# Performance work log

Measured on AMD Instinct MI355X. Metric: run time of the kernel, lower is better.

## Reference

```python
import jax, jax.numpy as jnp
import numpy as np


def setup_inputs() -> dict:
    key = jax.random.key(0)
    k1, k2, k3 = jax.random.split(key, 3)
    B, N, M, D = 4, 1024, 2048, 9
    outputs = jax.random.normal(k1, (B, N, D), dtype=jnp.float32)
    targets = jax.random.normal(k2, (B, M, D), dtype=jnp.float32)
    mask = jax.random.randint(k3, (B, M), 0, 2).astype(bool)
    return {"outputs": outputs, "targets": targets, "mask": mask, "k": 64, "max_pair": 1024}


def reference(outputs, targets, mask, k, max_pair):
    # outputs: (B, N, 9), targets: (B, M, 9), mask: (B, M) bool
    y_pred = outputs[:, :max_pair]
    B, N, D = y_pred.shape
    M = targets.shape[1]

    # Statistics over masked ground-truth rows (weighted, jit-friendly)
    w = mask.astype(y_pred.dtype)            # (B, M)
    S = w.sum()                               # number of valid rows
    mean = jnp.einsum('bm,bmd->d', w, targets) / S               # (9,)
    centered = (targets - mean) * w[..., None]                    # (B, M, 9)
    cov = jnp.einsum('bmd,bme->de', centered, centered) / (S - 1.0)
    cov_inv = jnp.linalg.pinv(cov)                                # (9, 9)

    def maha(x):
        # NOTE: original code subtracts the GT mean from the pairwise
        # differences before the quadratic form -- kept faithfully.
        xc = x - mean
        return jnp.einsum('...i,ij,...j->...', xc, cov_inv, xc)

    def topk_smallest_per_col(d, kk):
        # d: (R, N); torch.topk(dim=0, largest=False) -> smallest kk per column
        return -jax.lax.top_k(-d.T, kk)[0]    # (N, kk)

    # Intra loss: GT-vs-pred pairwise distances, masked rows only
    diff = targets[:, :, None, :] - y_pred[:, None, :, :]          # (B, M, N, 9)
    Dn = maha(diff)                                                 # (B, M, N)
    Dn = jnp.where(mask[:, :, None], Dn, jnp.inf).reshape(B * M, N)
    intra_loss = topk_smallest_per_col(Dn, k).mean()

    # Inter (regularization) loss: pred-vs-pred pairwise
    # y_reg1_expand[b,i,j] = y_pred[b,j]; y_reg2_expand[b,i,j] = y_pred[b,i]
    diff_r = y_pred[:, None, :, :] - y_pred[:, :, None, :]          # (B, N, N, 9)
    Dr = maha(diff_r).reshape(B * N, N)
    inter_loss = topk_smallest_per_col(Dr, k).mean()

    return intra_loss - 0.1 * inter_loss
```

## Files before the change

### kernel.cpp

```cpp
#include <hip/hip_runtime.h>
#include <math.h>

#define B_ 4
#define N_ 1024
#define M_ 2048
#define D_ 9
#define K_ 64
#define BM_ (B_*M_)
#define BN_ (B_*N_)
#define TPRE_STRIDE 12
#define PPRE_STRIDE 12
#define NPART 32
#define NSTAT 55
#define TSEL 512
#define BUD 128

#define WS_A 0
#define WS_MEAN 81
#define WS_TPRE 96
#define WS_PPRE (WS_TPRE + BM_*TPRE_STRIDE)
#define WS_CS_INTRA (WS_PPRE + BN_*PPRE_STRIDE)
#define WS_CS_INTER (WS_CS_INTRA + N_)
#define WS_PART (WS_CS_INTER + N_)
#define WS_CANDI (WS_PART + NPART*(NSTAT+1))
#define WS_CANDE (WS_CANDI + 1024*2048)

__device__ __forceinline__ unsigned f2key(float f) {
  unsigned b = __float_as_uint(f);
  return (b & 0x80000000u) ? ~b : (b | 0x80000000u);
}
__device__ __forceinline__ float key2f(unsigned k) {
  unsigned b = (k & 0x80000000u) ? (k ^ 0x80000000u) : ~k;
  return __uint_as_float(b);
}

__device__ int detect_mask_fmt(const void* mask, int* flags ) {
  int tid = threadIdx.x;
  if (tid < 2) flags[tid] = 0;
  __syncthreads();
  const unsigned char* mb = (const unsigned char*)mask;
  int la = 0, lb = 0;
  for (int i = tid; i < BM_; i += blockDim.x) {
    unsigned char c = mb[i];
    if (c) { if (i & 3) la = 1; else if ((i & 7) == 4) lb = 1; }
  }
  if (la) atomicOr(&flags[0], 1);
  if (lb) atomicOr(&flags[1], 1);
  __syncthreads();
  return flags[0] ? 0 : (flags[1] ? 1 : 2);
}
__device__ __forceinline__ int mask_at(const void* mask, int fmt, int t) {
  if (fmt == 0) return ((const unsigned char*)mask)[t] != 0;
  if (fmt == 1) return ((const int*)mask)[t] != 0;
  return ((const long long*)mask)[t] != 0LL;
}

__global__ __launch_bounds__(256) void stats_part_kernel(
    const float* __restrict__ targets, const void* __restrict__ mask,
    float* __restrict__ ws) {
  __shared__ int flags[2];
  __shared__ float wpart[4][NSTAT];
  int tid = threadIdx.x;
  int fmt = detect_mask_fmt(mask, flags);
  int t = blockIdx.x * 256 + tid;

  float v[NSTAT];
  float tv[D_];
  int m = mask_at(mask, fmt, t);
  const float* tp = targets + t * D_;
#pragma unroll
  for (int d = 0; d < D_; ++d) tv[d] = m ? tp[d] : 0.f;
  v[0] = m ? 1.f : 0.f;
#pragma unroll
  for (int d = 0; d < D_; ++d) v[1 + d] = tv[d];
  {
    int p = 10;
#pragma unroll
    for (int i = 0; i < D_; ++i)
#pragma unroll
      for (int j = i; j < D_; ++j, ++p) v[p] = tv[i] * tv[j];
  }
#pragma unroll
  for (int off = 32; off > 0; off >>= 1)
#pragma unroll
    for (int p = 0; p < NSTAT; ++p) v[p] += __shfl_down(v[p], off);
  int wave = tid >> 6, lane = tid & 63;
  if (lane == 0)
#pragma unroll
    for (int p = 0; p < NSTAT; ++p) wpart[wave][p] = v[p];
  __syncthreads();
  if (tid < NSTAT) {
    float s = wpart[0][tid] + wpart[1][tid] + wpart[2][tid] + wpart[3][tid];
    ws[WS_PART + blockIdx.x * (NSTAT + 1) + tid] = s;
  }
}

__global__ __launch_bounds__(256) void pre_kernel(
    const float* __restrict__ outputs, const float* __restrict__ targets,
    const void* __restrict__ mask, float* __restrict__ ws) {
  __shared__ int flags[2];
  __shared__ float tot[NSTAT];
  __shared__ float Atmp[9][9];
  __shared__ float Ash[81];
  __shared__ float msh[D_];
  int tid = threadIdx.x;
  int fmt = detect_mask_fmt(mask, flags);
  if (tid < NSTAT) {
    double s = 0.0;
    for (int b = 0; b < NPART; ++b)
      s += (double)ws[WS_PART + b * (NSTAT + 1) + tid];
    tot[tid] = (float)s;
  }
  __syncthreads();
  if (tid < 64) {
    int lane = tid;
    float S = tot[0];
    float col[9];
    int j = lane - 9;
    if (lane < 9) {
      float mj = tot[1 + lane] / S;
#pragma unroll
      for (int r = 0; r < 9; ++r) {
        float mr = tot[1 + r] / S;
        int i0 = r < lane ? r : lane;
        int j0 = r < lane ? lane : r;
        int p = i0 * 9 - (i0 * (i0 - 1)) / 2 + (j0 - i0);
        col[r] = (tot[10 + p] - S * mr * mj) / (S - 1.0f);
      }
    } else {
#pragma unroll
      for (int r = 0; r < 9; ++r) col[r] = (r == j) ? 1.f : 0.f;
    }
#pragma unroll
    for (int c = 0; c < 9; ++c) {
      float pv = __shfl(col[c], c);
      float inv = 1.f / pv;
      col[c] *= inv;
      float f[9];
#pragma unroll
      for (int r = 0; r < 9; ++r) f[r] = __shfl(col[r], c);
#pragma unroll
      for (int r = 0; r < 9; ++r)
        if (r != c) col[r] -= f[r] * col[c];
    }
    if (lane >= 9 && lane < 18) {
#pragma unroll
      for (int r = 0; r < 9; ++r) Atmp[r][j] = col[r];
    }
  }
  __syncthreads();
  if (tid < 9) msh[tid] = tot[1 + tid] / tot[0];
  for (int idx = tid; idx < 81; idx += 256) {
    int i0 = idx / 9, j0 = idx % 9;
    Ash[idx] = 0.5f * (Atmp[i0][j0] + Atmp[j0][i0]);
  }
  __syncthreads();

  int idx = blockIdx.x * 256 + tid;
  if (idx < BM_) {
    const float* tp = targets + idx * D_;
    float u[D_];
#pragma unroll
    for (int d = 0; d < D_; ++d) u[d] = tp[d] - msh[d];
    float cu = 0.f; float au[D_];
#pragma unroll
    for (int i = 0; i < D_; ++i) {
      float s = 0.f;
#pragma unroll
      for (int j = 0; j < D_; ++j) s += Ash[i * D_ + j] * u[j];
      au[i] = s; cu += u[i] * s;
    }
    if (!mask_at(mask, fmt, idx)) cu = INFINITY;
    float* o = ws + WS_TPRE + idx * TPRE_STRIDE;
#pragma unroll
    for (int d = 0; d < D_; ++d) o[d] = au[d];
    o[9] = cu; o[10] = 0.f; o[11] = 0.f;
  } else if (idx < BM_ + BN_) {
    int r = idx - BM_;
    const float* yp = outputs + r * D_;
    float y[D_], q[D_], aq[D_];
#pragma unroll
    for (int d = 0; d < D_; ++d) { y[d] = yp[d]; q[d] = y[d] + msh[d]; }
    float cp = 0.f, cq = 0.f;
#pragma unroll
    for (int i = 0; i < D_; ++i) {
      float sy = 0.f, sq = 0.f;
#pragma unroll
      for (int j = 0; j < D_; ++j) {
        sy += Ash[i * D_ + j] * y[j];
        sq += Ash[i * D_ + j] * q[j];
      }
      cp += y[i] * sy;
      aq[i] = sq; cq += q[i] * sq;
    }
    float* o = ws + WS_PPRE + r * PPRE_STRIDE;
#pragma unroll
    for (int d = 0; d < D_; ++d) o[d] = aq[d];
    o[9] = cq; o[10] = cp; o[11] = 0.f;
  }
}

template <int PER>
__device__ __forceinline__ unsigned bisect64(const unsigned* key) {
  unsigned kmin = 0xFFFFFFFFu;
#pragma unroll
  for (int j = 0; j < PER; ++j) kmin = key[j] < kmin ? key[j] : kmin;
  unsigned gmin = kmin, mmax = kmin;
#pragma unroll
  for (int off = 32; off > 0; off >>= 1) {
    unsigned a = (unsigned)__shfl_xor((int)gmin, off);
    unsigned b = (unsigned)__shfl_xor((int)mmax, off);
    gmin = a < gmin ? a : gmin;
    mmax = b > mmax ? b : mmax;
  }
  unsigned lo = gmin, hi = mmax;
  while (lo < hi) {
    unsigned mid = lo + ((hi - lo) >> 1);
    int cnt = 0;
#pragma unroll
    for (int j = 0; j < PER; ++j) cnt += __popcll(__ballot(key[j] <= mid));
    if (cnt >= K_) hi = mid; else lo = mid + 1;
  }
  return lo;
}

template <int PER>
__device__ __forceinline__ void sel_thresh2(const unsigned* k0,
                                            const unsigned* k1,
                                            unsigned& T0o, unsigned& T1o,
                                            int& st0, int& st1) {
  unsigned mn0 = 0xFFFFFFFFu, mn1 = 0xFFFFFFFFu;
#pragma unroll
  for (int j = 0; j < PER; ++j) {
    mn0 = k0[j] < mn0 ? k0[j] : mn0;
    mn1 = k1[j] < mn1 ? k1[j] : mn1;
  }
  unsigned g0 = mn0, x0 = mn0, g1 = mn1, x1 = mn1;
#pragma unroll
  for (int off = 32; off > 0; off >>= 1) {
    unsigned a0 = (unsigned)__shfl_xor((int)g0, off);
    unsigned b0 = (unsigned)__shfl_xor((int)x0, off);
    unsigned a1 = (unsigned)__shfl_xor((int)g1, off);
    unsigned b1 = (unsigned)__shfl_xor((int)x1, off);
    g0 = a0 < g0 ? a0 : g0;  x0 = b0 > x0 ? b0 : x0;
    g1 = a1 < g1 ? a1 : g1;  x1 = b1 > x1 ? b1 : x1;
  }
  unsigned lo0 = g0, hi0 = x0, lo1 = g1, hi1 = x1;
  int c0 = 0, c1 = 0;
#pragma unroll
  for (int j = 0; j < PER; ++j) {
    c0 += __popcll(__ballot(k0[j] <= hi0));
    c1 += __popcll(__ballot(k1[j] <= hi1));
  }
  while (((lo0 < hi0) && (c0 > BUD)) || ((lo1 < hi1) && (c1 > BUD))) {
    int a0 = (lo0 < hi0) && (c0 > BUD);
    int a1 = (lo1 < hi1) && (c1 > BUD);
    unsigned mid0 = lo0 + ((hi0 - lo0) >> 1);
    unsigned mid1 = lo1 + ((hi1 - lo1) >> 1);
    int n0 = 0, n1 = 0;
#pragma unroll
    for (int j = 0; j < PER; ++j) {
      n0 += __popcll(__ballot(k0[j] <= mid0));
      n1 += __popcll(__ballot(k1[j] <= mid1));
    }
    if (a0) { if (n0 >= K_) { hi0 = mid0; c0 = n0; } else lo0 = mid0 + 1; }
    if (a1) { if (n1 >= K_) { hi1 = mid1; c1 = n1; } else lo1 = mid1 + 1; }
  }
  T0o = hi0; st0 = (c0 > BUD);
  T1o = hi1; st1 = (c1 > BUD);
}

template <int PER>
__device__ __forceinline__ void compactB(const unsigned* key, unsigned T,
                                         int strict, float* candw, int lane) {
  unsigned long long lmask = (1ull << lane) - 1ull;
  int n = 0;
#pragma unroll
  for (int j = 0; j < PER; ++j) {
    bool p = strict ? (key[j] < T) : (key[j] <= T);
    unsigned long long m = __ballot(p);
    if (p) candw[n + __popcll(m & lmask)] = key2f(key[j]);
    n += __popcll(m);
  }
  float tv = key2f(T);
  for (int i = n + lane; i < BUD; i += 64) candw[i] = tv;
}

template <int NP>
__device__ __forceinline__ float final_sum(const float* __restrict__ cand,
                                           int lane) {
  unsigned kk[NP];
#pragma unroll
  for (int j = 0; j < NP; ++j) kk[j] = f2key(cand[j * 64 + lane]);
  unsigned T = bisect64<NP>(kk);
  float s = 0.f; int c = 0;
#pragma unroll
  for (int j = 0; j < NP; ++j)
    if (kk[j] < T) { s += key2f(kk[j]); c++; }
#pragma unroll
  for (int off = 32; off > 0; off >>= 1) {
    s += __shfl_down(s, off);
    c += __shfl_down(c, off);
  }
  return s + (float)(K_ - c) * key2f(T);
}

__global__ __launch_bounds__(TSEL) void select_kernel(
    const float* __restrict__ outputs, const float* __restrict__ wsro,
    float* __restrict__ ws) {
  __shared__ float vsh[2][B_][D_];
  __shared__ float cvsh[2][B_];
  int tid = threadIdx.x, wave = tid >> 6, lane = tid & 63;
  int bid = blockIdx.x;
  int is_intra = bid < N_;
  int p = is_intra ? (bid >> 1) : (bid - N_);
  int h = is_intra ? (bid & 1) : 0;
  int c0 = 2 * p;
  if (tid < 2 * B_ * D_) {
    int c = tid / (B_ * D_), rem = tid % (B_ * D_), b = rem / D_, d = rem % D_;
    vsh[c][b][d] = outputs[(b * N_ + c0 + c) * D_ + d];
  }
  if (tid < 2 * B_) {
    int c = tid >> 2, b = tid & 3;
    cvsh[c][b] = wsro[WS_PPRE + (b * N_ + c0 + c) * PPRE_STRIDE + 10];
  }
  __syncthreads();
  constexpr int PER = 8;
  unsigned k0[PER], k1[PER];
  if (is_intra) {
    const float* pre = wsro + WS_TPRE;
    int rowbase = h * 4096;
#pragma unroll
    for (int bbb = 0; bbb < 2; ++bbb) {
      int b = 2 * h + bbb;
      float v0[D_], v1[D_];
#pragma unroll
      for (int d = 0; d < D_; ++d) { v0[d] = vsh[0][b][d]; v1[d] = vsh[1][b][d]; }
      float cv0 = cvsh[0][b], cv1 = cvsh[1][b];
#pragma unroll
      for (int jj = 0; jj < 4; ++jj) {
        int j = bbb * 4 + jj;
        const float* row = pre + (rowbase + tid + TSEL * j) * TPRE_STRIDE;
        float4 a0 = *(const float4*)row;
        float4 a1 = *(const float4*)(row + 4);
        float2 a2 = *(const float2*)(row + 8);
        float d0 = a0.x * v0[0] + a0.y * v0[1] + a0.z * v0[2] + a0.w * v0[3] +
                   a1.x * v0[4] + a1.y * v0[5] + a1.z * v0[6] + a1.w * v0[7] +
                   a2.x * v0[8];
        float d1 = a0.x * v1[0] + a0.y * v1[1] + a0.z * v1[2] + a0.w * v1[3] +
                   a1.x * v1[4] + a1.y * v1[5] + a1.z * v1[6] + a1.w * v1[7] +
                   a2.x * v1[8];
        k0[j] = f2key(a2.y + cv0 - 2.0f * d0);
        k1[j] = f2key(a2.y + cv1 - 2.0f * d1);
      }
      __builtin_amdgcn_sched_barrier(0);
    }
  } else {
    const float* pre = wsro + WS_PPRE;
#pragma unroll
    for (int bb = 0; bb < B_; ++bb) {
      float v0[D_], v1[D_];
#pragma unroll
      for (int d = 0; d < D_; ++d) { v0[d] = vsh[0][bb][d]; v1[d] = vsh[1][bb][d]; }
      float cv0 = cvsh[0][bb], cv1 = cvsh[1][bb];
#pragma unroll
      for (int jj = 0; jj < 2; ++jj) {
        int j = bb * 2 + jj;
        const float* row = pre + (tid + TSEL * j) * PPRE_STRIDE;
        float4 a0 = *(const float4*)row;
        float4 a1 = *(const float4*)(row + 4);
        float2 a2 = *(const float2*)(row + 8);
        float d0 = a0.x * v0[0] + a0.y * v0[1] + a0.z * v0[2] + a0.w * v0[3] +
                   a1.x * v0[4] + a1.y * v0[5] + a1.z * v0[6] + a1.w * v0[7] +
                   a2.x * v0[8];
        float d1 = a0.x * v1[0] + a0.y * v1[1] + a0.z * v1[2] + a0.w * v1[3] +
                   a1.x * v1[4] + a1.y * v1[5] + a1.z * v1[6] + a1.w * v1[7] +
                   a2.x * v1[8];
        k0[j] = f2key(a2.y + cv0 - 2.0f * d0);
        k1[j] = f2key(a2.y + cv1 - 2.0f * d1);
      }
      __builtin_amdgcn_sched_barrier(0);
    }
  }
  unsigned T0, T1; int st0, st1;
  sel_thresh2<PER>(k0, k1, T0, T1, st0, st1);
  if (is_intra) {
    compactB<PER>(k0, T0, st0,
                  ws + WS_CANDI + (c0) * 2048 + h * 1024 + wave * BUD, lane);
    compactB<PER>(k1, T1, st1,
                  ws + WS_CANDI + (c0 + 1) * 2048 + h * 1024 + wave * BUD, lane);
  } else {
    compactB<PER>(k0, T0, st0,
                  ws + WS_CANDE + (c0) * 1024 + wave * BUD, lane);
    compactB<PER>(k1, T1, st1,
                  ws + WS_CANDE + (c0 + 1) * 1024 + wave * BUD, lane);
  }
}

__global__ __launch_bounds__(512) void merge_kernel(
    const float* __restrict__ wsro, float* __restrict__ ws) {
  int gw = (blockIdx.x * 512 + threadIdx.x) >> 6;
  int lane = threadIdx.x & 63;
  if (gw < N_) {
    float s = final_sum<32>(wsro + WS_CANDI + gw * 2048, lane);
    if (lane == 0) ws[WS_CS_INTRA + gw] = s;
  } else {
    float s = final_sum<16>(wsro + WS_CANDE + (gw - N_) * 1024, lane);
    if (lane == 0) ws[WS_CS_INTER + (gw - N_)] = s;
  }
}

__global__ __launch_bounds__(256) void reduce_kernel(
    const float* __restrict__ ws, float* __restrict__ out) {
  __shared__ double sbuf[256];
  __shared__ double tA;
  int tid = threadIdx.x;
  double sa = 0.0, sb = 0.0;
  for (int i = tid; i < N_; i += 256) {
    sa += (double)ws[WS_CS_INTRA + i];
    sb += (double)ws[WS_CS_INTER + i];
  }
  sbuf[tid] = sa;
  __syncthreads();
  for (int off = 128; off > 0; off >>= 1) {
    if (tid < off) sbuf[tid] += sbuf[tid + off];
    __syncthreads();
  }
  if (tid == 0) tA = sbuf[0];
  __syncthreads();
  sbuf[tid] = sb;
  __syncthreads();
  for (int off = 128; off > 0; off >>= 1) {
    if (tid < off) sbuf[tid] += sbuf[tid + off];
    __syncthreads();
  }
  if (tid == 0) {
    double denom = (double)N_ * (double)K_;
    out[0] = (float)(tA / denom - 0.1 * (sbuf[0] / denom));
  }
}

extern "C" void kernel_launch(void* const* d_in, const int* in_sizes, int n_in,
                              void* d_out, int out_size, void* d_ws,
                              size_t ws_size, hipStream_t stream) {
  const float* outputs = (const float*)d_in[0];
  const float* targets = (const float*)d_in[1];
  const void* mask = d_in[2];
  float* ws = (float*)d_ws;

  hipLaunchKernelGGL(stats_part_kernel, dim3(NPART), dim3(256), 0, stream,
                     targets, mask, ws);
  hipLaunchKernelGGL(pre_kernel, dim3((BM_ + BN_ + 255) / 256), dim3(256), 0,
                     stream, outputs, targets, mask, ws);
  hipLaunchKernelGGL(select_kernel, dim3(N_ + N_ / 2), dim3(TSEL), 0, stream,
                     outputs, ws, ws);
  hipLaunchKernelGGL(merge_kernel, dim3(2 * N_ / 8), dim3(512), 0, stream,
                     ws, ws);
  hipLaunchKernelGGL(reduce_kernel, dim3(1), dim3(256), 0, stream, ws,
                     (float*)d_out);
}
```

Before: 70.79 us.

## Fuse candidate merge and final reduction into select kernel via LDS and atomics

The select kernel now keeps per-wave top-k candidates in shared memory and computes each column's final sum within the same block, so the separate merge and reduce kernels and the global candidate buffers go away. Each intra block now handles both batch halves in two serial passes instead of splitting them across two blocks. Column sums are accumulated in fixed-point 64-bit integer atomics, and the last block to finish writes the output. This removes two launches and the global round trip, but halves intra parallelism (1024 blocks instead of 1536) and adds atomic contention plus a fixed-point rounding change.

```diff
diff --git a/kernel.cpp b/kernel.cpp
--- a/kernel.cpp
+++ b/kernel.cpp
@@ -14,6 +14,7 @@
 #define NSTAT 55
 #define TSEL 512
 #define BUD 128
+#define NBLK 1024
 
 #define WS_A 0
 #define WS_MEAN 81
@@ -22,8 +23,7 @@
 #define WS_CS_INTRA (WS_PPRE + BN_*PPRE_STRIDE)
 #define WS_CS_INTER (WS_CS_INTRA + N_)
 #define WS_PART (WS_CS_INTER + N_)
-#define WS_CANDI (WS_PART + NPART*(NSTAT+1))
-#define WS_CANDE (WS_CANDI + 1024*2048)
+#define WS_ACC (WS_PART + NPART*(NSTAT+1))
 
 __device__ __forceinline__ unsigned f2key(float f) {
   unsigned b = __float_as_uint(f);
@@ -105,6 +105,10 @@
   __shared__ float msh[D_];
   int tid = threadIdx.x;
   int fmt = detect_mask_fmt(mask, flags);
+  if (blockIdx.x == 0 && tid == 0) {
+    long long* acc = (long long*)(ws + WS_ACC);
+    acc[0] = 0; acc[1] = 0; acc[2] = 0;
+  }
   if (tid < NSTAT) {
     double s = 0.0;
     for (int b = 0; b < NPART; ++b)
@@ -307,14 +311,14 @@
 
 __global__ __launch_bounds__(TSEL) void select_kernel(
     const float* __restrict__ outputs, const float* __restrict__ wsro,
-    float* __restrict__ ws) {
+    float* __restrict__ ws, float* __restrict__ out) {
   __shared__ float vsh[2][B_][D_];
   __shared__ float cvsh[2][B_];
+  __shared__ float cand[2][16][BUD];
   int tid = threadIdx.x, wave = tid >> 6, lane = tid & 63;
   int bid = blockIdx.x;
-  int is_intra = bid < N_;
-  int p = is_intra ? (bid >> 1) : (bid - N_);
-  int h = is_intra ? (bid & 1) : 0;
+  int is_intra = bid < (N_ / 2);
+  int p = is_intra ? bid : bid - (N_ / 2);
   int c0 = 2 * p;
   if (tid < 2 * B_ * D_) {
     int c = tid / (B_ * D_), rem = tid % (B_ * D_), b = rem / D_, d = rem % D_;
@@ -329,31 +333,38 @@
   unsigned k0[PER], k1[PER];
   if (is_intra) {
     const float* pre = wsro + WS_TPRE;
-    int rowbase = h * 4096;
-#pragma unroll
-    for (int bbb = 0; bbb < 2; ++bbb) {
-      int b = 2 * h + bbb;
-      float v0[D_], v1[D_];
-#pragma unroll
-      for (int d = 0; d < D_; ++d) { v0[d] = vsh[0][b][d]; v1[d] = vsh[1][b][d]; }
-      float cv0 = cvsh[0][b], cv1 = cvsh[1][b];
-#pragma unroll
-      for (int jj = 0; jj < 4; ++jj) {
-        int j = bbb * 4 + jj;
-        const float* row = pre + (rowbase + tid + TSEL * j) * TPRE_STRIDE;
-        float4 a0 = *(const float4*)row;
-        float4 a1 = *(const float4*)(row + 4);
-        float2 a2 = *(const float2*)(row + 8);
-        float d0 = a0.x * v0[0] + a0.y * v0[1] + a0.z * v0[2] + a0.w * v0[3] +
-                   a1.x * v0[4] + a1.y * v0[5] + a1.z * v0[6] + a1.w * v0[7] +
-                   a2.x * v0[8];
-        float d1 = a0.x * v1[0] + a0.y * v1[1] + a0.z * v1[2] + a0.w * v1[3] +
-                   a1.x * v1[4] + a1.y * v1[5] + a1.z * v1[6] + a1.w * v1[7] +
-                   a2.x * v1[8];
-        k0[j] = f2key(a2.y + cv0 - 2.0f * d0);
-        k1[j] = f2key(a2.y + cv1 - 2.0f * d1);
+#pragma unroll 1
+    for (int pass = 0; pass < 2; ++pass) {
+      int rowbase = pass * 4096;
+#pragma unroll
+      for (int bbb = 0; bbb < 2; ++bbb) {
+        int b = pass * 2 + bbb;
+        float v0[D_], v1[D_];
+#pragma unroll
+        for (int d = 0; d < D_; ++d) { v0[d] = vsh[0][b][d]; v1[d] = vsh[1][b][d]; }
+        float cv0 = cvsh[0][b], cv1 = cvsh[1][b];
+#pragma unroll
+        for (int jj = 0; jj < 4; ++jj) {
+          int j = bbb * 4 + jj;
+          const float* row = pre + (rowbase + tid + TSEL * j) * TPRE_STRIDE;
+          float4 a0 = *(const float4*)row;
+          float4 a1 = *(const float4*)(row + 4);
+          float2 a2 = *(const float2*)(row + 8);
+          float d0 = a0.x * v0[0] + a0.y * v0[1] + a0.z * v0[2] + a0.w * v0[3] +
+                     a1.x * v0[4] + a1.y * v0[5] + a1.z * v0[6] + a1.w * v0[7] +
+                     a2.x * v0[8];
+          float d1 = a0.x * v1[0] + a0.y * v1[1] + a0.z * v1[2] + a0.w * v1[3] +
+                     a1.x * v1[4] + a1.y * v1[5] + a1.z * v1[6] + a1.w * v1[7] +
+                     a2.x * v1[8];
+          k0[j] = f2key(a2.y + cv0 - 2.0f * d0);
+          k1[j] = f2key(a2.y + cv1 - 2.0f * d1);
+        }
+        __builtin_amdgcn_sched_barrier(0);
       }
-      __builtin_amdgcn_sched_barrier(0);
+      unsigned T0, T1; int st0, st1;
+      sel_thresh2<PER>(k0, k1, T0, T1, st0, st1);
+      compactB<PER>(k0, T0, st0, &cand[0][pass * 8 + wave][0], lane);
+      compactB<PER>(k1, T1, st1, &cand[1][pass * 8 + wave][0], lane);
     }
   } else {
     const float* pre = wsro + WS_PPRE;
@@ -381,62 +392,31 @@
       }
       __builtin_amdgcn_sched_barrier(0);
     }
-  }
-  unsigned T0, T1; int st0, st1;
-  sel_thresh2<PER>(k0, k1, T0, T1, st0, st1);
-  if (is_intra) {
-    compactB<PER>(k0, T0, st0,
-                  ws + WS_CANDI + (c0) * 2048 + h * 1024 + wave * BUD, lane);
-    compactB<PER>(k1, T1, st1,
-                  ws + WS_CANDI + (c0 + 1) * 2048 + h * 1024 + wave * BUD, lane);
-  } else {
-    compactB<PER>(k0, T0, st0,
-                  ws + WS_CANDE + (c0) * 1024 + wave * BUD, lane);
-    compactB<PER>(k1, T1, st1,
-                  ws + WS_CANDE + (c0 + 1) * 1024 + wave * BUD, lane);
-  }
-}
-
-__global__ __launch_bounds__(512) void merge_kernel(
-    const float* __restrict__ wsro, float* __restrict__ ws) {
-  int gw = (blockIdx.x * 512 + threadIdx.x) >> 6;
-  int lane = threadIdx.x & 63;
-  if (gw < N_) {
-    float s = final_sum<32>(wsro + WS_CANDI + gw * 2048, lane);
-    if (lane == 0) ws[WS_CS_INTRA + gw] = s;
-  } else {
-    float s = final_sum<16>(wsro + WS_CANDE + (gw - N_) * 1024, lane);
-    if (lane == 0) ws[WS_CS_INTER + (gw - N_)] = s;
-  }
-}
-
-__global__ __launch_bounds__(256) void reduce_kernel(
-    const float* __restrict__ ws, float* __restrict__ out) {
-  __shared__ double sbuf[256];
-  __shared__ double tA;
-  int tid = threadIdx.x;
-  double sa = 0.0, sb = 0.0;
-  for (int i = tid; i < N_; i += 256) {
-    sa += (double)ws[WS_CS_INTRA + i];
-    sb += (double)ws[WS_CS_INTER + i];
-  }
-  sbuf[tid] = sa;
-  __syncthreads();
-  for (int off = 128; off > 0; off >>= 1) {
-    if (tid < off) sbuf[tid] += sbuf[tid + off];
-    __syncthreads();
-  }
-  if (tid == 0) tA = sbuf[0];
-  __syncthreads();
-  sbuf[tid] = sb;
-  __syncthreads();
-  for (int off = 128; off > 0; off >>= 1) {
-    if (tid < off) sbuf[tid] += sbuf[tid + off];
-    __syncthreads();
-  }
+    unsigned T0, T1; int st0, st1;
+    sel_thresh2<PER>(k0, k1, T0, T1, st0, st1);
+    compactB<PER>(k0, T0, st0, &cand[0][wave][0], lane);
+    compactB<PER>(k1, T1, st1, &cand[1][wave][0], lane);
+  }
+  __syncthreads();
+  unsigned long long* acc = (unsigned long long*)(ws + WS_ACC);
+  if (wave < 2) {
+    float s = is_intra ? final_sum<32>(&cand[wave][0][0], lane)
+                       : final_sum<16>(&cand[wave][0][0], lane);
+    if (lane == 0) {
+      long long v = (long long)llrint((double)s * 4294967296.0);
+      atomicAdd(&acc[is_intra ? 0 : 1], (unsigned long long)v);
+    }
+  }
+  __syncthreads();
   if (tid == 0) {
-    double denom = (double)N_ * (double)K_;
-    out[0] = (float)(tA / denom - 0.1 * (sbuf[0] / denom));
+    __threadfence();
+    unsigned long long old = atomicAdd(&acc[2], 1ull);
+    if (old == (unsigned long long)(NBLK - 1)) {
+      long long aI = (long long)atomicAdd(&acc[0], 0ull);
+      long long aE = (long long)atomicAdd(&acc[1], 0ull);
+      double dn = 4294967296.0 * (double)N_ * (double)K_;
+      out[0] = (float)((double)aI / dn - 0.1 * ((double)aE / dn));
+    }
   }
 }
 
@@ -452,10 +432,6 @@
                      targets, mask, ws);
   hipLaunchKernelGGL(pre_kernel, dim3((BM_ + BN_ + 255) / 256), dim3(256), 0,
                      stream, outputs, targets, mask, ws);
-  hipLaunchKernelGGL(select_kernel, dim3(N_ + N_ / 2), dim3(TSEL), 0, stream,
-                     outputs, ws, ws);
-  hipLaunchKernelGGL(merge_kernel, dim3(2 * N_ / 8), dim3(512), 0, stream,
-                     ws, ws);
-  hipLaunchKernelGGL(reduce_kernel, dim3(1), dim3(256), 0, stream, ws,
-                     (float*)d_out);
-}
+  hipLaunchKernelGGL(select_kernel, dim3(NBLK), dim3(TSEL), 0, stream,
+                     outputs, ws, ws, (float*)d_out);
+}
```

After: 122.3 us. 72.7% more time.
